# Kernel optimization log

Hardware: AMD Instinct MI355X
Metric: run time of the kernel (lower is better)

Reference implementation:

```python
import jax, jax.numpy as jnp
from jax import lax
import numpy as np

B, C, H, W = 4, 256, 64, 64
O, KH, KW = 256, 3, 3
STR, PAD, DIL = 1, 1, 1
K = KH * KW
EPS = 1e-5


def setup_inputs() -> dict:
    key = jax.random.key(0)
    ks = jax.random.split(key, 8)
    fan = 1.0 / np.sqrt(C * KH * KW)
    return {
        "input_x": jax.random.normal(ks[0], (B, C, H, W), jnp.float32),
        # offset-generating conv (DeformConv2dPack style): 2*K channels of (dy, dx)
        "w_offset": jax.random.normal(ks[1], (2 * K, C, KH, KW), jnp.float32) * 0.01,
        "b_offset": jnp.zeros((2 * K,), jnp.float32),
        # deformable conv weight / bias
        "weight": jax.random.normal(ks[2], (O, C, KH, KW), jnp.float32) * fan,
        "bias": jax.random.normal(ks[3], (O,), jnp.float32) * 0.01,
        # BatchNorm2d params + running stats (inference mode)
        "gamma": jax.random.normal(ks[4], (O,), jnp.float32) * 0.1 + 1.0,
        "beta": jax.random.normal(ks[5], (O,), jnp.float32) * 0.1,
        "run_mean": jax.random.normal(ks[6], (O,), jnp.float32) * 0.1,
        "run_var": jax.random.uniform(ks[7], (O,), jnp.float32, 0.5, 1.5),
    }


def _bilinear_sample(img, y, x):
    """img: [B,C,H,W]; y,x: [B,K,Ho,Wo] float sample coords. Zero outside."""
    y0 = jnp.floor(y)
    x0 = jnp.floor(x)
    ly = y - y0
    lx = x - x0
    y0i = y0.astype(jnp.int32)
    x0i = x0.astype(jnp.int32)
    y1i = y0i + 1
    x1i = x0i + 1

    def valid(yi, xi):
        return ((yi >= 0) & (yi < H) & (xi >= 0) & (xi < W)).astype(img.dtype)

    # per-corner interpolation weights, zeroed when the corner is out of bounds
    w00 = (1 - ly) * (1 - lx) * valid(y0i, x0i)
    w01 = (1 - ly) * lx * valid(y0i, x1i)
    w10 = ly * (1 - lx) * valid(y1i, x0i)
    w11 = ly * lx * valid(y1i, x1i)

    y0c = jnp.clip(y0i, 0, H - 1)
    y1c = jnp.clip(y1i, 0, H - 1)
    x0c = jnp.clip(x0i, 0, W - 1)
    x1c = jnp.clip(x1i, 0, W - 1)

    gather = jax.vmap(lambda im, yi, xi: im[:, yi, xi])  # -> [B,C,K,Ho,Wo]
    out = gather(img, y0c, x0c) * w00[:, None]
    out = out + gather(img, y0c, x1c) * w01[:, None]
    out = out + gather(img, y1c, x0c) * w10[:, None]
    out = out + gather(img, y1c, x1c) * w11[:, None]
    return out  # [B,C,K,Ho,Wo]


def reference(input_x, w_offset, b_offset, weight, bias, gamma, beta, run_mean, run_var):
    # 1) generate offsets with a regular conv (DeformConv2dPack conv_offset)
    offset = lax.conv_general_dilated(
        input_x, w_offset, (STR, STR), [(PAD, PAD), (PAD, PAD)],
        rhs_dilation=(DIL, DIL), dimension_numbers=("NCHW", "OIHW", "NCHW"))
    offset = offset + b_offset[None, :, None, None]  # [B, 2K, Ho, Wo]
    Ho, Wo = offset.shape[2], offset.shape[3]
    off = offset.reshape(B, K, 2, Ho, Wo)
    dy, dx = off[:, :, 0], off[:, :, 1]  # [B,K,Ho,Wo]

    # 2) base sampling grid for each kernel tap
    ky, kx = jnp.meshgrid(jnp.arange(KH), jnp.arange(KW), indexing="ij")
    base_y = (jnp.arange(Ho) * STR - PAD)[None, :, None] + (ky.reshape(-1) * DIL)[:, None, None]
    base_x = (jnp.arange(Wo) * STR - PAD)[None, None, :] + (kx.reshape(-1) * DIL)[:, None, None]
    y = base_y.astype(input_x.dtype) + dy  # [B,K,Ho,Wo]
    x = base_x.astype(input_x.dtype) + dx

    # 3) bilinear-sampled im2col then dense contraction
    sampled = _bilinear_sample(input_x, y, x)  # [B,C,K,Ho,Wo]
    out = jnp.einsum("bckhw,ock->bohw", sampled, weight.reshape(O, C, K))
    out = out + bias[None, :, None, None]

    # 4) BatchNorm (inference, running stats) + ReLU
    inv = gamma / jnp.sqrt(run_var + EPS)
    out = out * inv[None, :, None, None] + (beta - run_mean * inv)[None, :, None, None]
    return jax.nn.relu(out)
```

## Files before the change

### kernel.cpp

```cpp
#include <hip/hip_runtime.h>
#include <math.h>

typedef __attribute__((ext_vector_type(8))) short b8;
typedef __attribute__((ext_vector_type(4))) float f4;
typedef float f4u __attribute__((ext_vector_type(4), aligned(4)));
typedef _Float16 h8 __attribute__((ext_vector_type(8)));
typedef _Float16 h2 __attribute__((ext_vector_type(2)));

#define XT2   0
#define OF2   2097152
#define WH2   2392064
#define WL2   2428928
#define AF2   3571712
#define BF2   3866624

#define BARRIER_RELAX() do {                                   \
    asm volatile("s_waitcnt lgkmcnt(0)" ::: "memory");         \
    __builtin_amdgcn_s_barrier();                              \
  } while (0)

__device__ inline ushort f2bf(float f) {
  uint u = __float_as_uint(f);
  return (ushort)((u + 0x7FFFu + ((u >> 16) & 1u)) >> 16);
}
__device__ inline h2 u2h2(uint u) { union { uint u; h2 h; } x; x.u = u; return x.h; }
__device__ inline uint h22u(h2 h) { union { uint u; h2 h; } x; x.h = h; return x.u; }
__device__ inline uint duph(float f) {
  union { _Float16 h; ushort u; } x; x.h = (_Float16)f;
  return ((uint)x.u << 16) | x.u;
}

__global__ __launch_bounds__(256) void prep0_k(
    const float* __restrict__ wof, const float* __restrict__ bias,
    const float* __restrict__ gamma, const float* __restrict__ beta,
    const float* __restrict__ mean, const float* __restrict__ var,
    float* __restrict__ ws) {
  const int tid = blockIdx.x * 256 + threadIdx.x;
  ((f4*)(ws + OF2))[tid] = f4{0.f, 0.f, 0.f, 0.f};
  if (tid < 256) {
    const float iv = gamma[tid] * rsqrtf(var[tid] + 1e-5f);
    ws[BF2 + tid] = bias[tid] * iv + beta[tid] - mean[tid] * iv;
  }
  if (tid < 9216) {
    const int l2  = tid & 63;
    const int mt  = (tid >> 6) & 1;
    const int i2  = tid >> 7;
    const int cg2 = i2 / 9;
    const int kk2 = i2 - cg2 * 9;
    const int oc  = (mt << 4) + (l2 & 15);
    const int cb2 = (cg2 << 5) + ((l2 >> 4) << 3);
    b8 ph, pl;
#pragma unroll
    for (int j = 0; j < 8; ++j) {
      const float v = (oc < 18) ? wof[((oc << 8) + cb2 + j) * 9 + kk2] : 0.f;
      const ushort h = f2bf(v);
      const float hf = __uint_as_float((uint)h << 16);
      ph[j] = (short)h;
      pl[j] = (short)f2bf(v - hf);
    }
    *(b8*)((short*)(ws + WH2) + tid * 8) = ph;
    *(b8*)((short*)(ws + WL2) + tid * 8) = pl;
  }
}

__global__ __launch_bounds__(256, 4) void mid_k(
    const float* __restrict__ x, const float* __restrict__ w,
    const float* __restrict__ gamma, const float* __restrict__ var,
    float* __restrict__ ws) {
  __shared__ __align__(16) ushort Xh[3][66][40];
  __shared__ __align__(16) ushort Xl[3][66][40];
  const int bid = blockIdx.x;
  const int t   = threadIdx.x;

  if (bid >= 3072) {
    const int tid = (bid - 3072) * 256 + t;
    const int l  = tid & 63;
    const int ot = (tid >> 6) & 15;
    const int f  = tid >> 10;
    const int o  = (ot << 4) + (l & 15);
    const float inv = gamma[o] * rsqrtf(var[o] + 1e-5f);
    const int s  = f & 1;
    const int g  = f >> 1;
    const int cw = g / 9;
    const int kk = g - cw * 9;
    const int cb = (cw << 6) + (s << 5) + ((l >> 4) << 3);
    h8 pk;
#pragma unroll
    for (int j = 0; j < 8; ++j)
      pk[j] = (_Float16)(w[((o << 8) + cb + j) * 9 + kk] * inv);
    *(h8*)((_Float16*)(ws + AF2) + tid * 8) = pk;
    return;
  }

  const int r = bid % 3;
  const int g = bid / 3;
  if (r != 2) {
    const int id  = ((g << 1) + r) * 256 + t;
    const int p   = id & 4095;
    const int cg8 = (id >> 12) & 31;
    const int b   = id >> 17;
    const float* xp = x + (((long)(b * 256 + cg8 * 8)) << 12) + p;
    _Float16* xt = (_Float16*)(ws + XT2);
    h8 pk;
#pragma unroll
    for (int j = 0; j < 8; ++j) pk[j] = (_Float16)xp[(long)j << 12];
    *(h8*)(xt + ((((long)(b << 12) + p)) << 8) + (cg8 << 3)) = pk;
    return;
  }

  const int q   = g >> 8;
  const int b   = (g >> 6) & 3;
  const int ho  = g & 63;
  const int l   = t & 63;
  const int wv  = t >> 6;
  const short* afh = (const short*)(ws + WH2);
  const short* afl = (const short*)(ws + WL2);

  for (int u = t; u < 240; u += 256) {
    const int row = u / 80, rem = u % 80;
    const int col = (rem >= 40) ? 65 : 0;
    const int c   = rem % 40;
    Xh[row][col][c] = 0;
    Xl[row][col][c] = 0;
  }

  f4 acc[2];
  acc[0] = f4{0.f, 0.f, 0.f, 0.f};
  acc[1] = f4{0.f, 0.f, 0.f, 0.f};

  const int cidx = t >> 3;
  const int j8   = t & 7;
  const float* xc = x + ((long)b << 20) + ((long)cidx << 12);
  const int col = (wv << 4) + (l & 15);
  const int qc  = (l >> 4) << 3;

  for (int it = 0; it < 2; ++it) {
    const int cg = (q << 1) + it;
    __syncthreads();
    const float* xg = xc + ((long)(cg << 5) << 12);
#pragma unroll
    for (int rep = 0; rep < 6; ++rep) {
      const int fi   = (rep << 3) + j8;
      const int row  = fi >> 4;
      const int colf = (fi & 15) << 2;
      const int y = ho - 1 + row;
      f4u v = {0.f, 0.f, 0.f, 0.f};
      if (y >= 0 && y <= 63) v = *(const f4u*)(xg + (y << 6) + colf);
#pragma unroll
      for (int qq = 0; qq < 4; ++qq) {
        const ushort h = f2bf(v[qq]);
        const float hf = __uint_as_float((uint)h << 16);
        Xh[row][colf + 1 + qq][cidx] = h;
        Xl[row][colf + 1 + qq][cidx] = f2bf(v[qq] - hf);
      }
    }
    __syncthreads();
#pragma unroll
    for (int kk = 0; kk < 9; ++kk) {
      const int ky = kk / 3, kx = kk - ky * 3;
      const int i  = cg * 9 + kk;
      const b8 ah0 = *(const b8*)(afh + ((((i << 1) + 0) << 6) + l) * 8);
      const b8 ah1 = *(const b8*)(afh + ((((i << 1) + 1) << 6) + l) * 8);
      const b8 al0 = *(const b8*)(afl + ((((i << 1) + 0) << 6) + l) * 8);
      const b8 al1 = *(const b8*)(afl + ((((i << 1) + 1) << 6) + l) * 8);
      const b8 bh = *(const b8*)&Xh[ky][col + kx][qc];
      const b8 bl = *(const b8*)&Xl[ky][col + kx][qc];
      acc[0] = __builtin_amdgcn_mfma_f32_16x16x32_bf16(ah0, bh, acc[0], 0, 0, 0);
      acc[0] = __builtin_amdgcn_mfma_f32_16x16x32_bf16(ah0, bl, acc[0], 0, 0, 0);
      acc[0] = __builtin_amdgcn_mfma_f32_16x16x32_bf16(al0, bh, acc[0], 0, 0, 0);
      acc[1] = __builtin_amdgcn_mfma_f32_16x16x32_bf16(ah1, bh, acc[1], 0, 0, 0);
      acc[1] = __builtin_amdgcn_mfma_f32_16x16x32_bf16(ah1, bl, acc[1], 0, 0, 0);
      acc[1] = __builtin_amdgcn_mfma_f32_16x16x32_bf16(al1, bh, acc[1], 0, 0, 0);
    }
  }

  const int wo = col;
  const int q4 = (l >> 4) << 2;
#pragma unroll
  for (int mt = 0; mt < 2; ++mt)
#pragma unroll
    for (int rr = 0; rr < 4; ++rr) {
      const int oc = (mt << 4) + q4 + rr;
      if (oc < 18)
        atomicAdd(&ws[OF2 + ((b * 18 + oc) << 12) + (ho << 6) + wo],
                  acc[mt][rr]);
    }
}

__global__ __launch_bounds__(1024, 1) void deform_gemm_f16b(
    const float* __restrict__ ws, const float* __restrict__ bof,
    float* __restrict__ out) {
  __shared__ __align__(16) uint Bs[4][64][32];
  __shared__ uint4 dW[576];
  __shared__ int4  dP[576];

  const int t     = threadIdx.x;
  const int bid   = blockIdx.x;
  const int xcd   = bid & 7;
  const int batch = xcd >> 1;
  const int half  = xcd & 1;
  const int j     = bid >> 3;
  const int sp0   = (half << 11) + (j << 6);
  const int l     = t & 63;
  const int wv    = t >> 6;

  const int sl  = t & 511;
  const int swv = sl >> 6;
  const int hh  = t >> 9;
  const int sn  = ((swv & 3) << 4) | (l & 15);
  const int cg8 = ((swv >> 2) << 2) | (l >> 4);
  const uint* xtu = (const uint*)(ws + XT2) + ((long)batch << 19);
  const _Float16* af = (const _Float16*)(ws + AF2);

  for (int u = t; u < 576; u += 1024) {
    const int kk = u >> 6, s = u & 63;
    const int sp = sp0 + s;
    const int ho = sp >> 6, wo = sp & 63;
    const int ky = kk / 3, kx = kk - ky * 3;
    const float dy =
        ws[OF2 + ((batch * 18 + (kk << 1)) << 12) + sp] + bof[kk << 1];
    const float dx =
        ws[OF2 + ((batch * 18 + (kk << 1) + 1) << 12) + sp] + bof[(kk << 1) + 1];
    const float py = (float)(ho - 1 + ky) + dy;
    const float px = (float)(wo - 1 + kx) + dx;
    const float y0f = floorf(py), x0f = floorf(px);
    const float ly = py - y0f, lx = px - x0f;
    const int y0 = (int)y0f, x0 = (int)x0f;
    const int y1 = y0 + 1, x1 = x0 + 1;
    const float vy0 = (y0 >= 0 && y0 < 64) ? 1.f : 0.f;
    const float vy1 = (y1 >= 0 && y1 < 64) ? 1.f : 0.f;
    const float vx0 = (x0 >= 0 && x0 < 64) ? 1.f : 0.f;
    const float vx1 = (x1 >= 0 && x1 < 64) ? 1.f : 0.f;
    const int y0c = min(max(y0, 0), 63), y1c = min(max(y1, 0), 63);
    const int x0c = min(max(x0, 0), 63), x1c = min(max(x1, 0), 63);
    uint4 wv4;
    wv4.x = duph((1.f - ly) * (1.f - lx) * vy0 * vx0);
    wv4.y = duph((1.f - ly) * lx * vy0 * vx1);
    wv4.z = duph(ly * (1.f - lx) * vy1 * vx0);
    wv4.w = duph(ly * lx * vy1 * vx1);
    int4 pv;
    pv.x = (y0c << 6) + x0c;
    pv.y = (y0c << 6) + x1c;
    pv.z = (y1c << 6) + x0c;
    pv.w = (y1c << 6) + x1c;
    dW[u] = wv4;
    dP[u] = pv;
  }
  __syncthreads();

  f4 acc[4];
#pragma unroll
  for (int nt = 0; nt < 4; ++nt) acc[nt] = f4{0.f, 0.f, 0.f, 0.f};

  uint2 cset0[4], cset1[4];
  uint4 w0v, w1v, wq; int4 pq;
  h8 aA[2], aN[2];
  int kkd, kkg, cwg;

#define FRDD(W_, P_, KK_) do { const int u_ = ((KK_) << 6) + sn;             \
    W_ = dW[u_]; P_ = dP[u_]; } while (0)

#define FGATH(DST_, P_) do {                                                 \
    const int co_ = (cwg << 5) + (cg8 << 2) + (hh << 1);                     \
    DST_[0] = *(const uint2*)(xtu + ((P_).x << 7) + co_);                    \
    DST_[1] = *(const uint2*)(xtu + ((P_).y << 7) + co_);                    \
    DST_[2] = *(const uint2*)(xtu + ((P_).z << 7) + co_);                    \
    DST_[3] = *(const uint2*)(xtu + ((P_).w << 7) + co_);                    \
  } while (0)

#define FCOMB(CS_, WV_, BUF_) do {                                           \
    const h2 wc0_ = u2h2((WV_).x), wc1_ = u2h2((WV_).y);                     \
    const h2 wc2_ = u2h2((WV_).z), wc3_ = u2h2((WV_).w);                     \
    uint2 r_;                                                                \
    r_.x = h22u(u2h2(CS_[0].x) * wc0_ + u2h2(CS_[1].x) * wc1_ +              \
                u2h2(CS_[2].x) * wc2_ + u2h2(CS_[3].x) * wc3_);              \
    r_.y = h22u(u2h2(CS_[0].y) * wc0_ + u2h2(CS_[1].y) * wc1_ +              \
                u2h2(CS_[2].y) * wc2_ + u2h2(CS_[3].y) * wc3_);              \
    *(uint2*)&Bs[BUF_][sn][((cg8 ^ (sn & 7)) << 2) + (hh << 1)] = r_;        \
  } while (0)

#define FLOADA(I_, DST_) do {                                                \
    _Pragma("unroll")                                                        \
    for (int s = 0; s < 2; ++s) {                                            \
      const int f_ = ((I_) << 1) + s;                                        \
      DST_[s] = *(const h8*)(af + ((((f_ << 4) + wv) << 6) + l) * 8);        \
    }                                                                        \
  } while (0)

#define FMFMA(AC_, BUF_) do {                                                \
    h8 bB_[4][2];                                                            \
    _Pragma("unroll")                                                        \
    for (int nt = 0; nt < 4; ++nt)                                           \
      _Pragma("unroll")                                                      \
      for (int s = 0; s < 2; ++s) {                                          \
        const int snr_ = (nt << 4) + (l & 15);                               \
        const int ph_  = (((s << 2) + (l >> 4)) ^ (snr_ & 7)) << 2;          \
        bB_[nt][s] = *(const h8*)&Bs[BUF_][snr_][ph_];                       \
      }                                                                      \
    _Pragma("unroll")                                                        \
    for (int nt = 0; nt < 4; ++nt) {                                         \
      acc[nt] = __builtin_amdgcn_mfma_f32_16x16x32_f16(                      \
          AC_[0], bB_[nt][0], acc[nt], 0, 0, 0);                             \
      acc[nt] = __builtin_amdgcn_mfma_f32_16x16x32_f16(                      \
          AC_[1], bB_[nt][1], acc[nt], 0, 0, 0);                             \
    }                                                                        \
  } while (0)

#define FBODY2(J_) do {                                                      \
    const int je_ = (J_);                                                    \
    if (je_ < 33) { w0v = wq; FGATH(cset0, pq);                              \
      kkg++; if (kkg == 9) { kkg = 0; cwg++; } }                             \
    if (je_ < 32) { FRDD(wq, pq, kkd); kkd = (kkd == 8) ? 0 : kkd + 1; }     \
    __builtin_amdgcn_s_setprio(1);                                           \
    FMFMA(aA, (je_ & 3));                                                    \
    __builtin_amdgcn_s_setprio(0);                                           \
    if (je_ < 35) FLOADA(je_ + 1, aN);                                       \
    if (je_ < 34) FCOMB(cset1, w1v, ((je_ + 2) & 3));                        \
    const int jo_ = (J_) + 1;                                                \
    if (jo_ < 33) { w1v = wq; FGATH(cset1, pq);                              \
      kkg++; if (kkg == 9) { kkg = 0; cwg++; } }                             \
    if (jo_ < 32) { FRDD(wq, pq, kkd); kkd = (kkd == 8) ? 0 : kkd + 1; }     \
    __builtin_amdgcn_s_setprio(1);                                           \
    FMFMA(aN, (jo_ & 3));                                                    \
    __builtin_amdgcn_s_setprio(0);                                           \
    if (jo_ < 35) FLOADA(jo_ + 1, aA);                                       \
    if (jo_ < 34) FCOMB(cset0, w0v, ((jo_ + 2) & 3));                        \
    BARRIER_RELAX();                                                         \
  } while (0)

  {
    uint4 wA, wB; int4 pA;
    cwg = 0;
    FRDD(wA, pA, 0); FGATH(cset0, pA);
    FRDD(wB, pA, 1); FGATH(cset1, pA);
    FCOMB(cset0, wA, 0);
    FCOMB(cset1, wB, 1);
    FRDD(w1v, pA, 2); FGATH(cset1, pA);
    FRDD(wq, pq, 3);
    FLOADA(0, aA);
    kkd = 4; kkg = 3;
  }
  BARRIER_RELAX();

  for (int i = 0; i < 36; i += 2) FBODY2(i);

  const float* bfold = ws + BF2;
  const int quad = l >> 4;
  {
    const int ob = (wv << 4) + (quad << 2);
    const f4 bf = *(const f4*)&bfold[ob];
#pragma unroll
    for (int nt = 0; nt < 4; ++nt) {
      const int sp = sp0 + (nt << 4) + (l & 15);
#pragma unroll
      for (int rr = 0; rr < 4; ++rr) {
        out[(((batch << 8) + ob + rr) << 12) + sp] =
            fmaxf(acc[nt][rr] + bf[rr], 0.f);
      }
    }
  }
}

extern "C" void kernel_launch(void* const* d_in, const int* in_sizes, int n_in,
                              void* d_out, int out_size, void* d_ws, size_t ws_size,
                              hipStream_t stream) {
  const float* x     = (const float*)d_in[0];
  const float* wof   = (const float*)d_in[1];
  const float* bof   = (const float*)d_in[2];
  const float* w     = (const float*)d_in[3];
  const float* bias  = (const float*)d_in[4];
  const float* gamma = (const float*)d_in[5];
  const float* beta  = (const float*)d_in[6];
  const float* mean  = (const float*)d_in[7];
  const float* var   = (const float*)d_in[8];
  float* out = (float*)d_out;
  float* ws  = (float*)d_ws;

  hipLaunchKernelGGL(prep0_k, dim3(288), dim3(256), 0, stream,
                     wof, bias, gamma, beta, mean, var, ws);
  hipLaunchKernelGGL(mid_k, dim3(3360), dim3(256), 0, stream,
                     x, w, gamma, var, ws);
  hipLaunchKernelGGL(deform_gemm_f16b, dim3(256), dim3(1024), 0, stream,
                     ws, bof, out);
}
```

Before: 180.1 us.

## Split gather by thread half across taps and widen loads to 16 bytes

Each thread half (hh) now handles alternate kernel taps instead of splitting channels within a tap. Gathers become 16-byte uint4 loads covering 8 channels, and each thread writes a 16-byte LDS store per step. The pipeline is restructured into pair bodies that issue one gather/combine per two MFMA stages, so each barrier covers two k-chunks. This cuts the number of gather instructions and barriers per chunk, at the cost of more registers per thread and a more intricate buffer indexing that depends on hh.

```diff
diff --git a/kernel.cpp b/kernel.cpp
--- a/kernel.cpp
+++ b/kernel.cpp
@@ -203,10 +203,9 @@
   const int sp0   = (half << 11) + (j << 6);
   const int l     = t & 63;
   const int wv    = t >> 6;
-
-  const int sl  = t & 511;
-  const int swv = sl >> 6;
-  const int hh  = t >> 9;
+  const int hh    = t >> 9;
+
+  const int swv = (t & 511) >> 6;
   const int sn  = ((swv & 3) << 4) | (l & 15);
   const int cg8 = ((swv >> 2) << 2) | (l >> 4);
   const uint* xtu = (const uint*)(ws + XT2) + ((long)batch << 19);
@@ -252,31 +251,35 @@
 #pragma unroll
   for (int nt = 0; nt < 4; ++nt) acc[nt] = f4{0.f, 0.f, 0.f, 0.f};
 
-  uint2 cset0[4], cset1[4];
+  uint4 csetA[4], csetB[4];
   uint4 w0v, w1v, wq; int4 pq;
   h8 aA[2], aN[2];
-  int kkd, kkg, cwg;
+  int dkk, gkk2, gcw;
 
 #define FRDD(W_, P_, KK_) do { const int u_ = ((KK_) << 6) + sn;             \
     W_ = dW[u_]; P_ = dP[u_]; } while (0)
 
 #define FGATH(DST_, P_) do {                                                 \
-    const int co_ = (cwg << 5) + (cg8 << 2) + (hh << 1);                     \
-    DST_[0] = *(const uint2*)(xtu + ((P_).x << 7) + co_);                    \
-    DST_[1] = *(const uint2*)(xtu + ((P_).y << 7) + co_);                    \
-    DST_[2] = *(const uint2*)(xtu + ((P_).z << 7) + co_);                    \
-    DST_[3] = *(const uint2*)(xtu + ((P_).w << 7) + co_);                    \
+    const int co_ = (gcw << 5) + (cg8 << 2);                                 \
+    DST_[0] = *(const uint4*)(xtu + ((P_).x << 7) + co_);                    \
+    DST_[1] = *(const uint4*)(xtu + ((P_).y << 7) + co_);                    \
+    DST_[2] = *(const uint4*)(xtu + ((P_).z << 7) + co_);                    \
+    DST_[3] = *(const uint4*)(xtu + ((P_).w << 7) + co_);                    \
   } while (0)
 
 #define FCOMB(CS_, WV_, BUF_) do {                                           \
     const h2 wc0_ = u2h2((WV_).x), wc1_ = u2h2((WV_).y);                     \
     const h2 wc2_ = u2h2((WV_).z), wc3_ = u2h2((WV_).w);                     \
-    uint2 r_;                                                                \
+    uint4 r_;                                                                \
     r_.x = h22u(u2h2(CS_[0].x) * wc0_ + u2h2(CS_[1].x) * wc1_ +              \
                 u2h2(CS_[2].x) * wc2_ + u2h2(CS_[3].x) * wc3_);              \
     r_.y = h22u(u2h2(CS_[0].y) * wc0_ + u2h2(CS_[1].y) * wc1_ +              \
                 u2h2(CS_[2].y) * wc2_ + u2h2(CS_[3].y) * wc3_);              \
-    *(uint2*)&Bs[BUF_][sn][((cg8 ^ (sn & 7)) << 2) + (hh << 1)] = r_;        \
+    r_.z = h22u(u2h2(CS_[0].z) * wc0_ + u2h2(CS_[1].z) * wc1_ +              \
+                u2h2(CS_[2].z) * wc2_ + u2h2(CS_[3].z) * wc3_);              \
+    r_.w = h22u(u2h2(CS_[0].w) * wc0_ + u2h2(CS_[1].w) * wc1_ +              \
+                u2h2(CS_[2].w) * wc2_ + u2h2(CS_[3].w) * wc3_);              \
+    *(uint4*)&Bs[BUF_][sn][(cg8 ^ (sn & 7)) << 2] = r_;                      \
   } while (0)
 
 #define FLOADA(I_, DST_) do {                                                \
@@ -306,43 +309,41 @@
     }                                                                        \
   } while (0)
 
-#define FBODY2(J_) do {                                                      \
-    const int je_ = (J_);                                                    \
-    if (je_ < 33) { w0v = wq; FGATH(cset0, pq);                              \
-      kkg++; if (kkg == 9) { kkg = 0; cwg++; } }                             \
-    if (je_ < 32) { FRDD(wq, pq, kkd); kkd = (kkd == 8) ? 0 : kkd + 1; }     \
+#define PBODY(P_, CC_, WC_, CN_, WN_) do {                                   \
+    if ((P_) < 16) { WN_ = wq; FGATH(CN_, pq);                               \
+      gkk2 += 2; if (gkk2 >= 9) { gkk2 -= 9; gcw++; } }                      \
+    if ((P_) < 15) { FRDD(wq, pq, dkk); dkk += 2; if (dkk >= 9) dkk -= 9; }  \
     __builtin_amdgcn_s_setprio(1);                                           \
-    FMFMA(aA, (je_ & 3));                                                    \
+    FMFMA(aA, (((P_) << 1) & 3));                                            \
     __builtin_amdgcn_s_setprio(0);                                           \
-    if (je_ < 35) FLOADA(je_ + 1, aN);                                       \
-    if (je_ < 34) FCOMB(cset1, w1v, ((je_ + 2) & 3));                        \
-    const int jo_ = (J_) + 1;                                                \
-    if (jo_ < 33) { w1v = wq; FGATH(cset1, pq);                              \
-      kkg++; if (kkg == 9) { kkg = 0; cwg++; } }                             \
-    if (jo_ < 32) { FRDD(wq, pq, kkd); kkd = (kkd == 8) ? 0 : kkd + 1; }     \
+    if ((P_) < 17) FLOADA(((P_) << 1) + 2, aA);                              \
     __builtin_amdgcn_s_setprio(1);                                           \
-    FMFMA(aN, (jo_ & 3));                                                    \
+    FMFMA(aN, ((((P_) << 1) + 1) & 3));                                      \
     __builtin_amdgcn_s_setprio(0);                                           \
-    if (jo_ < 35) FLOADA(jo_ + 1, aA);                                       \
-    if (jo_ < 34) FCOMB(cset0, w0v, ((jo_ + 2) & 3));                        \
+    if ((P_) < 17) { FLOADA(((P_) << 1) + 3, aN);                            \
+      FCOMB(CC_, WC_, ((((P_) << 1) + 2 + hh) & 3)); }                       \
     BARRIER_RELAX();                                                         \
   } while (0)
 
   {
-    uint4 wA, wB; int4 pA;
-    cwg = 0;
-    FRDD(wA, pA, 0); FGATH(cset0, pA);
-    FRDD(wB, pA, 1); FGATH(cset1, pA);
-    FCOMB(cset0, wA, 0);
-    FCOMB(cset1, wB, 1);
-    FRDD(w1v, pA, 2); FGATH(cset1, pA);
-    FRDD(wq, pq, 3);
+    uint4 wA; int4 pA;
+    gcw = 0;
+    FRDD(wA, pA, hh);
+    FGATH(csetB, pA);
+    FCOMB(csetB, wA, hh);
+    FRDD(w1v, pA, hh + 2);
+    FGATH(csetA, pA);
+    FRDD(wq, pq, hh + 4);
     FLOADA(0, aA);
-    kkd = 4; kkg = 3;
+    FLOADA(1, aN);
+    dkk = hh + 6; gkk2 = hh + 4;
   }
   BARRIER_RELAX();
 
-  for (int i = 0; i < 36; i += 2) FBODY2(i);
+  for (int P = 0; P < 18; P += 2) {
+    PBODY(P,     csetA, w1v, csetB, w0v);
+    PBODY(P + 1, csetB, w0v, csetA, w1v);
+  }
 
   const float* bfold = ws + BF2;
   const int quad = l >> 4;
```

After: 150.2 us. -16.6%, faster.
